# Kernel tuning notes

Measured on AMD Instinct MI355X. Metric: run time of the kernel, lower is better.

The kernel has to match this reference:

```python
import jax, jax.numpy as jnp
import numpy as np

N_NODES = 100000
N_EDGES = 1600000
IN_DIM, HID_DIM, OUT_DIM = 256, 128, 64


def setup_inputs() -> dict:
    key = jax.random.key(0)
    k1, k2, k3, k4, k5 = jax.random.split(key, 5)
    h = jax.random.normal(k1, (N_NODES, IN_DIM), dtype=jnp.float32)
    src = jax.random.randint(k2, (N_EDGES,), 0, N_NODES, dtype=jnp.int32)
    dst = jax.random.randint(k3, (N_EDGES,), 0, N_NODES, dtype=jnp.int32)
    # Glorot-uniform weights like DGL GraphConv defaults, zero bias
    lim1 = np.sqrt(6.0 / (IN_DIM + HID_DIM))
    lim2 = np.sqrt(6.0 / (HID_DIM + OUT_DIM))
    W1 = jax.random.uniform(k4, (IN_DIM, HID_DIM), jnp.float32, -lim1, lim1)
    W2 = jax.random.uniform(k5, (HID_DIM, OUT_DIM), jnp.float32, -lim2, lim2)
    b1 = jnp.zeros((HID_DIM,), jnp.float32)
    b2 = jnp.zeros((OUT_DIM,), jnp.float32)
    return {"h": h, "W1": W1, "b1": b1, "W2": W2, "b2": b2, "src": src, "dst": dst}


def _graph_conv(h, W, b, src, dst):
    # DGL GraphConv, norm='both', allow_zero_in_degree=True:
    #   out = D_in^{-1/2} A D_out^{-1/2} h W + b  (degrees clamped to min 1)
    ones = jnp.ones(src.shape[0], dtype=h.dtype)
    deg_out = jnp.clip(jax.ops.segment_sum(ones, src, num_segments=N_NODES), 1.0, None)
    feat = h * (deg_out ** -0.5)[:, None]
    # in_feats > out_feats for both layers -> multiply by W first (DGL order)
    feat = feat @ W  # [N, out]
    agg = jax.ops.segment_sum(feat[src], dst, num_segments=N_NODES)  # SpMM
    deg_in = jnp.clip(jax.ops.segment_sum(ones, dst, num_segments=N_NODES), 1.0, None)
    return agg * (deg_in ** -0.5)[:, None] + b


def reference(h, W1, b1, W2, b2, src, dst):
    # dropout is identity in eval mode (training=False)
    x = _graph_conv(h, W1, b1, src, dst)
    x = jax.nn.relu(x)
    logits = _graph_conv(x, W2, b2, src, dst)
    return jax.nn.softmax(logits, axis=1), logits
```

## Files before the change

kernel.cpp:

```cpp
#include <hip/hip_runtime.h>
#include <cstdio>

#define NN 100000
#define NE 1600000
#define IN_DIM 256
#define HID_DIM 128
#define OUT_DIM 64

#define EPB 4096
#define NBLK ((NE + EPB - 1) / EPB)
#define FBSH 7
#define FBN 128
#define NFB 782
#define CAP 2560
#define PREP_ELEMS (HID_DIM * IN_DIM + OUT_DIM * HID_DIM)
#define PREP_BLKS ((PREP_ELEMS + 127) / 128)

typedef short s8v __attribute__((ext_vector_type(8)));
typedef float f4v __attribute__((ext_vector_type(4)));
typedef _Float16 h2v __attribute__((ext_vector_type(2)));
typedef unsigned u32x4 __attribute__((ext_vector_type(4)));
typedef unsigned short u16x4 __attribute__((ext_vector_type(4)));
typedef unsigned short u16x8 __attribute__((ext_vector_type(8)));

__device__ __forceinline__ unsigned short f2bf(float f) {
    unsigned u = __builtin_bit_cast(unsigned, f);
    u += 0x7FFFu + ((u >> 16) & 1u);
    return (unsigned short)(u >> 16);
}
__device__ __forceinline__ unsigned short f2h(float f) {
    return __builtin_bit_cast(unsigned short, (_Float16)f);
}
__device__ __forceinline__ h2v bch2(unsigned w) { return __builtin_bit_cast(h2v, w); }

__global__ __launch_bounds__(256) void scat1_kernel(const int* __restrict__ src,
                                                    const int* __restrict__ dst,
                                                    unsigned short* __restrict__ cnt2dD,
                                                    unsigned short* __restrict__ cnt2dS) {
    __shared__ unsigned hbD[NFB], hbS[NFB];
    const int t = threadIdx.x;
    for (int i = t; i < NFB; i += 256) { hbD[i] = 0u; hbS[i] = 0u; }
    __syncthreads();
    const int base = blockIdx.x * EPB;
    int n = NE - base; if (n > EPB) n = EPB;
    for (int i = t; i < n; i += 256) {
        atomicAdd(&hbD[dst[base + i] >> FBSH], 1u);
        atomicAdd(&hbS[src[base + i] >> FBSH], 1u);
    }
    __syncthreads();
    const size_t row = (size_t)blockIdx.x * NFB;
    for (int i = t; i < NFB; i += 256) {
        cnt2dD[row + i] = (unsigned short)hbD[i];
        cnt2dS[row + i] = (unsigned short)hbS[i];
    }
}

__global__ __launch_bounds__(128) void scanCprep_kernel(unsigned short* __restrict__ cnt2dD,
                                                        unsigned short* __restrict__ cnt2dS,
                                                        unsigned* __restrict__ btotD,
                                                        unsigned* __restrict__ btotS,
                                                        const float* __restrict__ W1,
                                                        const float* __restrict__ W2,
                                                        unsigned short* __restrict__ W1t,
                                                        unsigned short* __restrict__ W2t) {
    const int g = blockIdx.x;
    if (g >= 2 * NFB) {
        int i = (g - 2 * NFB) * 128 + threadIdx.x;
        if (i < HID_DIM * IN_DIM) {
            int n = i >> 8, k = i & 255;
            W1t[i] = f2bf(W1[k * HID_DIM + n]);
        } else if (i < PREP_ELEMS) {
            int m = i - HID_DIM * IN_DIM;
            int n = m >> 7, k = m & 127;
            W2t[m] = f2bf(W2[k * OUT_DIM + n]);
        }
        return;
    }
    __shared__ unsigned sc[128];
    unsigned short* arr = (g < NFB) ? cnt2dD : cnt2dS;
    unsigned* btot = (g < NFB) ? btotD : btotS;
    const int b = (g < NFB) ? g : g - NFB;
    const int t = threadIdx.x;
    unsigned v[4];
    unsigned s = 0;
#pragma unroll
    for (int i = 0; i < 4; ++i) {
        int blk = t * 4 + i;
        unsigned x = (blk < NBLK) ? (unsigned)arr[(size_t)blk * NFB + b] : 0u;
        v[i] = s;
        s += x;
    }
    sc[t] = s;
    __syncthreads();
    for (int o = 1; o < 128; o <<= 1) {
        unsigned add = (t >= o) ? sc[t - o] : 0u;
        __syncthreads();
        sc[t] += add;
        __syncthreads();
    }
    unsigned incl = sc[t];
    unsigned excl = incl - s;
#pragma unroll
    for (int i = 0; i < 4; ++i) {
        int blk = t * 4 + i;
        if (blk < NBLK) arr[(size_t)blk * NFB + b] = (unsigned short)(excl + v[i]);
    }
    if (t == 127) btot[b] = incl;
}

__global__ __launch_bounds__(256) void scat2_kernel(const int* __restrict__ src,
                                                    const int* __restrict__ dst,
                                                    const unsigned short* __restrict__ ofsD,
                                                    const unsigned short* __restrict__ ofsS,
                                                    unsigned* __restrict__ ebufD,
                                                    unsigned char* __restrict__ ebufS) {
    __shared__ unsigned curD[NFB], curS[NFB];
    const int t = threadIdx.x;
    const size_t row = (size_t)blockIdx.x * NFB;
    for (int i = t; i < NFB; i += 256) {
        curD[i] = (unsigned)i * CAP + (unsigned)ofsD[row + i];
        curS[i] = (unsigned)i * CAP + (unsigned)ofsS[row + i];
    }
    __syncthreads();
    const int base = blockIdx.x * EPB;
    int n = NE - base; if (n > EPB) n = EPB;
    for (int i = t; i < n; i += 256) {
        int d = dst[base + i];
        int s = src[base + i];
        unsigned pD = atomicAdd(&curD[d >> FBSH], 1u);
        ebufD[pD] = ((unsigned)(d & 127) << 17) | (unsigned)s;
        unsigned pS = atomicAdd(&curS[s >> FBSH], 1u);
        ebufS[pS] = (unsigned char)(s & 127);
    }
}

__global__ __launch_bounds__(256) void bsortc_kernel(const unsigned* __restrict__ ebufD,
                                                     const unsigned* __restrict__ btotD,
                                                     const unsigned char* __restrict__ ebufS,
                                                     const unsigned* __restrict__ btotS,
                                                     int* __restrict__ csr,
                                                     unsigned* __restrict__ rsinfo,
                                                     float* __restrict__ dsin,
                                                     unsigned* __restrict__ cnt_out) {
    __shared__ unsigned hn[FBN];
    __shared__ unsigned sc[FBN];
    __shared__ unsigned cur[FBN];
    const int b = blockIdx.x;
    const int t = threadIdx.x;
    const unsigned e0 = (unsigned)b * CAP;
    const unsigned e1 = e0 + btotD[b];
    if (t < FBN) hn[t] = 0u;
    __syncthreads();
    for (unsigned j = e0 + t; j < e1; j += 256) atomicAdd(&hn[(ebufD[j] >> 17) & 127u], 1u);
    __syncthreads();
    unsigned cnt_t = (t < FBN) ? hn[t] : 0u;
    if (t < FBN) sc[t] = cnt_t;
    __syncthreads();
    for (int o = 1; o < FBN; o <<= 1) {
        unsigned add = (t < FBN && t >= o) ? sc[t - o] : 0u;
        __syncthreads();
        if (t < FBN) sc[t] += add;
        __syncthreads();
    }
    if (t < FBN) {
        unsigned excl = sc[t] - cnt_t;
        cur[t] = e0 + excl;
        int node = (b << FBSH) + t;
        if (node < NN) {
            rsinfo[node] = ((e0 + excl) << 10) | (cnt_t & 1023u);
            dsin[node] = rsqrtf((float)(cnt_t ? cnt_t : 1u));
        }
    }
    __syncthreads();
    for (unsigned j = e0 + t; j < e1; j += 256) {
        unsigned pk = ebufD[j];
        unsigned pos = atomicAdd(&cur[(pk >> 17) & 127u], 1u);
        csr[pos] = (int)(pk & 0x1FFFFu);
    }
    __syncthreads();
    if (t < FBN) hn[t] = 0u;
    __syncthreads();
    const unsigned nS = btotS[b];
    for (unsigned j = t; j < nS; j += 256) atomicAdd(&hn[ebufS[e0 + j]], 1u);
    __syncthreads();
    if (t < FBN) {
        int node = (b << FBSH) + t;
        if (node < NN) cnt_out[node] = hn[t];
    }
}

__global__ __launch_bounds__(256) void gemm1_kernel(const float* __restrict__ h,
                                                    const unsigned short* __restrict__ W1t,
                                                    const unsigned* __restrict__ cnt_out,
                                                    unsigned short* __restrict__ feat1, int M) {
    __shared__ unsigned short sA[2][128][40];
    const int tid = threadIdx.x;
    const int lane = tid & 63;
    const int wave = tid >> 6;
    const int wm = wave >> 1, wn = wave & 1;
    const int m0 = blockIdx.x * 128;
    const int arow = tid >> 3;
    const int akq = tid & 7;

    f4v acc[4][4];
#pragma unroll
    for (int i = 0; i < 4; ++i)
#pragma unroll
        for (int j = 0; j < 4; ++j) acc[i][j] = (f4v)0.f;

    int mrow[4]; bool mok[4];
#pragma unroll
    for (int i = 0; i < 4; ++i) { mrow[i] = m0 + arow + i * 32; mok[i] = mrow[i] < M; }

    float4 pre[4];
#pragma unroll
    for (int i = 0; i < 4; ++i)
        pre[i] = mok[i] ? *reinterpret_cast<const float4*>(&h[(size_t)mrow[i] * IN_DIM + akq * 4])
                        : make_float4(0.f, 0.f, 0.f, 0.f);
#pragma unroll
    for (int i = 0; i < 4; ++i) {
        u16x4 p;
        p[0] = f2bf(pre[i].x); p[1] = f2bf(pre[i].y);
        p[2] = f2bf(pre[i].z); p[3] = f2bf(pre[i].w);
        *reinterpret_cast<u16x4*>(&sA[0][arow + i * 32][akq * 4]) = p;
    }
    __syncthreads();

    int cur = 0;
#pragma unroll
    for (int ks = 0; ks < 8; ++ks) {
        if (ks < 7) {
            const int k0n = (ks + 1) * 32;
#pragma unroll
            for (int i = 0; i < 4; ++i)
                pre[i] = mok[i] ? *reinterpret_cast<const float4*>(
                                      &h[(size_t)mrow[i] * IN_DIM + k0n + akq * 4])
                                : make_float4(0.f, 0.f, 0.f, 0.f);
        }
        s8v bfrag[4];
#pragma unroll
        for (int ni = 0; ni < 4; ++ni)
            bfrag[ni] = *reinterpret_cast<const s8v*>(
                &W1t[(size_t)(wn * 64 + ni * 16 + (lane & 15)) * IN_DIM + ks * 32 + (lane >> 4) * 8]);
        s8v afrag[4];
#pragma unroll
        for (int mi = 0; mi < 4; ++mi)
            afrag[mi] = *reinterpret_cast<const s8v*>(
                &sA[cur][wm * 64 + mi * 16 + (lane & 15)][(lane >> 4) * 8]);
#pragma unroll
        for (int ni = 0; ni < 4; ++ni)
#pragma unroll
            for (int mi = 0; mi < 4; ++mi)
                acc[mi][ni] = __builtin_amdgcn_mfma_f32_16x16x32_bf16(afrag[mi], bfrag[ni], acc[mi][ni], 0, 0, 0);
        if (ks < 7) {
#pragma unroll
            for (int i = 0; i < 4; ++i) {
                u16x4 p;
                p[0] = f2bf(pre[i].x); p[1] = f2bf(pre[i].y);
                p[2] = f2bf(pre[i].z); p[3] = f2bf(pre[i].w);
                *reinterpret_cast<u16x4*>(&sA[cur ^ 1][arow + i * 32][akq * 4]) = p;
            }
        }
        __syncthreads();
        cur ^= 1;
    }
#pragma unroll
    for (int mi = 0; mi < 4; ++mi) {
#pragma unroll
        for (int j = 0; j < 4; ++j) {
            int row = m0 + wm * 64 + mi * 16 + (lane >> 4) * 4 + j;
            if (row < M) {
                unsigned cdeg = cnt_out[row];
                float s = rsqrtf((float)(cdeg ? cdeg : 1u));
#pragma unroll
                for (int ni = 0; ni < 4; ++ni) {
                    int col = wn * 64 + ni * 16 + (lane & 15);
                    feat1[(size_t)row * HID_DIM + col] = f2h(acc[mi][ni][j] * s);
                }
            }
        }
    }
}

__global__ __launch_bounds__(256) void gemm2_kernel(const unsigned short* __restrict__ xs,
                                                    const unsigned short* __restrict__ W2t,
                                                    unsigned short* __restrict__ feat2, int M) {
    __shared__ unsigned short sA[2][128][40];
    const int tid = threadIdx.x;
    const int lane = tid & 63;
    const int wave = tid >> 6;
    const int wm = wave >> 1, wn = wave & 1;
    const int m0 = blockIdx.x * 128;

    f4v acc[4][2];
#pragma unroll
    for (int i = 0; i < 4; ++i)
#pragma unroll
        for (int j = 0; j < 2; ++j) acc[i][j] = (f4v)0.f;

    int srow[2], skq[2]; bool sok[2];
#pragma unroll
    for (int i = 0; i < 2; ++i) {
        int idx = tid + i * 256;
        srow[i] = idx >> 2; skq[i] = idx & 3;
        sok[i] = (m0 + srow[i]) < M;
    }

    u16x8 pre[2];
#pragma unroll
    for (int i = 0; i < 2; ++i)
        pre[i] = sok[i] ? *reinterpret_cast<const u16x8*>(
                              &xs[(size_t)(m0 + srow[i]) * HID_DIM + skq[i] * 8])
                        : (u16x8)0;
#pragma unroll
    for (int i = 0; i < 2; ++i)
        *reinterpret_cast<u16x8*>(&sA[0][srow[i]][skq[i] * 8]) = pre[i];
    __syncthreads();

    int cur = 0;
#pragma unroll
    for (int ks = 0; ks < 4; ++ks) {
        if (ks < 3) {
            const int k0n = (ks + 1) * 32;
#pragma unroll
            for (int i = 0; i < 2; ++i)
                pre[i] = sok[i] ? *reinterpret_cast<const u16x8*>(
                                      &xs[(size_t)(m0 + srow[i]) * HID_DIM + k0n + skq[i] * 8])
                                : (u16x8)0;
        }
        s8v bfrag[2];
#pragma unroll
        for (int ni = 0; ni < 2; ++ni)
            bfrag[ni] = *reinterpret_cast<const s8v*>(
                &W2t[(size_t)(wn * 32 + ni * 16 + (lane & 15)) * HID_DIM + ks * 32 + (lane >> 4) * 8]);
        s8v afrag[4];
#pragma unroll
        for (int mi = 0; mi < 4; ++mi)
            afrag[mi] = *reinterpret_cast<const s8v*>(
                &sA[cur][wm * 64 + mi * 16 + (lane & 15)][(lane >> 4) * 8]);
#pragma unroll
        for (int ni = 0; ni < 2; ++ni)
#pragma unroll
            for (int mi = 0; mi < 4; ++mi)
                acc[mi][ni] = __builtin_amdgcn_mfma_f32_16x16x32_bf16(afrag[mi], bfrag[ni], acc[mi][ni], 0, 0, 0);
        if (ks < 3) {
#pragma unroll
            for (int i = 0; i < 2; ++i)
                *reinterpret_cast<u16x8*>(&sA[cur ^ 1][srow[i]][skq[i] * 8]) = pre[i];
        }
        __syncthreads();
        cur ^= 1;
    }
#pragma unroll
    for (int mi = 0; mi < 4; ++mi)
#pragma unroll
        for (int ni = 0; ni < 2; ++ni) {
            int col = wn * 32 + ni * 16 + (lane & 15);
#pragma unroll
            for (int j = 0; j < 4; ++j) {
                int row = m0 + wm * 64 + mi * 16 + (lane >> 4) * 4 + j;
                if (row < M) feat2[(size_t)row * OUT_DIM + col] = f2h(acc[mi][ni][j]);
            }
        }
}

__global__ __launch_bounds__(256) void spmm1_kernel(const unsigned short* __restrict__ feat,
                                                    const int* __restrict__ csr,
                                                    const unsigned* __restrict__ rsinfo,
                                                    const float* __restrict__ dsin,
                                                    const unsigned* __restrict__ cnt_out,
                                                    const float* __restrict__ b1,
                                                    unsigned short* __restrict__ xs) {
    const int wave = threadIdx.x >> 6;
    const int lane = threadIdx.x & 63;
    const int node = blockIdx.x * 4 + wave;
    if (node >= NN) return;
    const unsigned info = rsinfo[node];
    unsigned j = info >> 10;
    int rem = (int)(info & 1023u);
    const int g = lane >> 4;
    const int c8 = (lane & 15) * 8;
    h2v acch[4];
#pragma unroll
    for (int i = 0; i < 4; ++i) acch[i] = (h2v)0;
    while (rem > 0) {
        const int take = rem < 64 ? rem : 64;
        const int idx = (lane < take) ? csr[j + lane] : 0;
        int e = 0;
        for (; e + 16 <= take; e += 16) {
            int s0 = __shfl(idx, e + g, 64);
            int s1 = __shfl(idx, e + 4 + g, 64);
            int s2 = __shfl(idx, e + 8 + g, 64);
            int s3 = __shfl(idx, e + 12 + g, 64);
            u32x4 v0 = *reinterpret_cast<const u32x4*>(&feat[(size_t)s0 * HID_DIM + c8]);
            u32x4 v1 = *reinterpret_cast<const u32x4*>(&feat[(size_t)s1 * HID_DIM + c8]);
            u32x4 v2 = *reinterpret_cast<const u32x4*>(&feat[(size_t)s2 * HID_DIM + c8]);
            u32x4 v3 = *reinterpret_cast<const u32x4*>(&feat[(size_t)s3 * HID_DIM + c8]);
#pragma unroll
            for (int k = 0; k < 4; ++k) {
                h2v t0 = bch2(v0[k]) + bch2(v1[k]);
                h2v t1 = bch2(v2[k]) + bch2(v3[k]);
                acch[k] += t0 + t1;
            }
        }
        for (; e + 4 <= take; e += 4) {
            int s0 = __shfl(idx, e + g, 64);
            u32x4 v0 = *reinterpret_cast<const u32x4*>(&feat[(size_t)s0 * HID_DIM + c8]);
#pragma unroll
            for (int k = 0; k < 4; ++k) acch[k] += bch2(v0[k]);
        }
        if (e < take) {
            int ei = e + g;
            int sl = ei < take ? ei : take - 1;
            int s0 = __shfl(idx, sl, 64);
            u32x4 v0 = *reinterpret_cast<const u32x4*>(&feat[(size_t)s0 * HID_DIM + c8]);
            if (ei < take) {
#pragma unroll
                for (int k = 0; k < 4; ++k) acch[k] += bch2(v0[k]);
            }
        }
        j += take; rem -= take;
    }
#pragma unroll
    for (int k = 0; k < 4; ++k) {
        unsigned w = __builtin_bit_cast(unsigned, acch[k]);
        acch[k] += bch2((unsigned)__shfl_xor((int)w, 16, 64));
        w = __builtin_bit_cast(unsigned, acch[k]);
        acch[k] += bch2((unsigned)__shfl_xor((int)w, 32, 64));
    }
    if (g == 0) {
        const float si = dsin[node];
        const unsigned co = cnt_out[node];
        const float so = rsqrtf((float)(co ? co : 1u));
        const float4 bb0 = *reinterpret_cast<const float4*>(&b1[c8]);
        const float4 bb1 = *reinterpret_cast<const float4*>(&b1[c8 + 4]);
        const float bv[8] = {bb0.x, bb0.y, bb0.z, bb0.w, bb1.x, bb1.y, bb1.z, bb1.w};
        u16x8 p;
#pragma unroll
        for (int k = 0; k < 4; ++k) {
            p[2 * k] = f2bf(fmaxf((float)acch[k][0] * si + bv[2 * k], 0.f) * so);
            p[2 * k + 1] = f2bf(fmaxf((float)acch[k][1] * si + bv[2 * k + 1], 0.f) * so);
        }
        *reinterpret_cast<u16x8*>(&xs[(size_t)node * HID_DIM + c8]) = p;
    }
}

__global__ __launch_bounds__(256) void spmm2_kernel(const unsigned short* __restrict__ feat2,
                                                    const int* __restrict__ csr,
                                                    const unsigned* __restrict__ rsinfo,
                                                    const float* __restrict__ dsin,
                                                    const float* __restrict__ b2,
                                                    float* __restrict__ out) {
    const int wave = threadIdx.x >> 6;
    const int lane = threadIdx.x & 63;
    const int node = blockIdx.x * 4 + wave;
    if (node >= NN) return;
    const unsigned info = rsinfo[node];
    unsigned j = info >> 10;
    int rem = (int)(info & 1023u);
    const int g = lane >> 3;
    const int c8 = (lane & 7) * 8;
    h2v acch[4];
#pragma unroll
    for (int i = 0; i < 4; ++i) acch[i] = (h2v)0;
    while (rem > 0) {
        const int take = rem < 64 ? rem : 64;
        const int idx = (lane < take) ? csr[j + lane] : 0;
        int e = 0;
        for (; e + 32 <= take; e += 32) {
            int s0 = __shfl(idx, e + g, 64);
            int s1 = __shfl(idx, e + 8 + g, 64);
            int s2 = __shfl(idx, e + 16 + g, 64);
            int s3 = __shfl(idx, e + 24 + g, 64);
            u32x4 v0 = *reinterpret_cast<const u32x4*>(&feat2[(size_t)s0 * OUT_DIM + c8]);
            u32x4 v1 = *reinterpret_cast<const u32x4*>(&feat2[(size_t)s1 * OUT_DIM + c8]);
            u32x4 v2 = *reinterpret_cast<const u32x4*>(&feat2[(size_t)s2 * OUT_DIM + c8]);
            u32x4 v3 = *reinterpret_cast<const u32x4*>(&feat2[(size_t)s3 * OUT_DIM + c8]);
#pragma unroll
            for (int k = 0; k < 4; ++k) {
                h2v t0 = bch2(v0[k]) + bch2(v1[k]);
                h2v t1 = bch2(v2[k]) + bch2(v3[k]);
                acch[k] += t0 + t1;
            }
        }
        for (; e + 16 <= take; e += 16) {
            int s0 = __shfl(idx, e + g, 64);
            int s1 = __shfl(idx, e + 8 + g, 64);
            u32x4 v0 = *reinterpret_cast<const u32x4*>(&feat2[(size_t)s0 * OUT_DIM + c8]);
            u32x4 v1 = *reinterpret_cast<const u32x4*>(&feat2[(size_t)s1 * OUT_DIM + c8]);
#pragma unroll
            for (int k = 0; k < 4; ++k) acch[k] += bch2(v0[k]) + bch2(v1[k]);
        }
        for (; e + 8 <= take; e += 8) {
            int s0 = __shfl(idx, e + g, 64);
            u32x4 v0 = *reinterpret_cast<const u32x4*>(&feat2[(size_t)s0 * OUT_DIM + c8]);
#pragma unroll
            for (int k = 0; k < 4; ++k) acch[k] += bch2(v0[k]);
        }
        if (e < take) {
            int ei = e + g;
            int sl = ei < take ? ei : take - 1;
            int s0 = __shfl(idx, sl, 64);
            u32x4 v0 = *reinterpret_cast<const u32x4*>(&feat2[(size_t)s0 * OUT_DIM + c8]);
            if (ei < take) {
#pragma unroll
                for (int k = 0; k < 4; ++k) acch[k] += bch2(v0[k]);
            }
        }
        j += take; rem -= take;
    }
#pragma unroll
    for (int k = 0; k < 4; ++k) {
        unsigned w = __builtin_bit_cast(unsigned, acch[k]);
        acch[k] += bch2((unsigned)__shfl_xor((int)w, 8, 64));
        w = __builtin_bit_cast(unsigned, acch[k]);
        acch[k] += bch2((unsigned)__shfl_xor((int)w, 16, 64));
        w = __builtin_bit_cast(unsigned, acch[k]);
        acch[k] += bch2((unsigned)__shfl_xor((int)w, 32, 64));
    }
    const float si = dsin[node];
    const float4 bb0 = *reinterpret_cast<const float4*>(&b2[c8]);
    const float4 bb1 = *reinterpret_cast<const float4*>(&b2[c8 + 4]);
    const float bv[8] = {bb0.x, bb0.y, bb0.z, bb0.w, bb1.x, bb1.y, bb1.z, bb1.w};
    float l[8];
#pragma unroll
    for (int k = 0; k < 4; ++k) {
        l[2 * k] = (float)acch[k][0] * si + bv[2 * k];
        l[2 * k + 1] = (float)acch[k][1] * si + bv[2 * k + 1];
    }
    float m = l[0];
#pragma unroll
    for (int i = 1; i < 8; ++i) m = fmaxf(m, l[i]);
    m = fmaxf(m, __shfl_xor(m, 1, 64));
    m = fmaxf(m, __shfl_xor(m, 2, 64));
    m = fmaxf(m, __shfl_xor(m, 4, 64));
    float ee[8];
    float s = 0.f;
#pragma unroll
    for (int i = 0; i < 8; ++i) { ee[i] = __expf(l[i] - m); s += ee[i]; }
    s += __shfl_xor(s, 1, 64);
    s += __shfl_xor(s, 2, 64);
    s += __shfl_xor(s, 4, 64);
    const float inv = 1.0f / s;
    if (lane < 8) {
        float4 p0 = make_float4(ee[0] * inv, ee[1] * inv, ee[2] * inv, ee[3] * inv);
        float4 p1 = make_float4(ee[4] * inv, ee[5] * inv, ee[6] * inv, ee[7] * inv);
        *reinterpret_cast<float4*>(&out[(size_t)node * OUT_DIM + c8]) = p0;
        *reinterpret_cast<float4*>(&out[(size_t)node * OUT_DIM + c8 + 4]) = p1;
        float4 q0 = make_float4(l[0], l[1], l[2], l[3]);
        float4 q1 = make_float4(l[4], l[5], l[6], l[7]);
        float* lg = &out[(size_t)NN * OUT_DIM + (size_t)node * OUT_DIM + c8];
        *reinterpret_cast<float4*>(lg) = q0;
        *reinterpret_cast<float4*>(lg + 4) = q1;
    }
}

static inline size_t align_up(size_t x, size_t a) { return (x + a - 1) & ~(a - 1); }

extern "C" void kernel_launch(void* const* d_in, const int* in_sizes, int n_in,
                              void* d_out, int out_size, void* d_ws, size_t ws_size,
                              hipStream_t stream) {
    (void)in_sizes; (void)n_in; (void)out_size;
    const float* h = (const float*)d_in[0];
    const float* W1 = (const float*)d_in[1];
    const float* b1 = (const float*)d_in[2];
    const float* W2 = (const float*)d_in[3];
    const float* b2 = (const float*)d_in[4];
    const int* src = (const int*)d_in[5];
    const int* dst = (const int*)d_in[6];
    float* out = (float*)d_out;

    char* ws = (char*)d_ws;
    size_t off = 0;
    auto alloc = [&](size_t bytes) {
        void* p = (void*)(ws + off);
        off = align_up(off + bytes, 512);
        return p;
    };
    unsigned* cnt_out = (unsigned*)alloc(NN * 4);
    unsigned short* cnt2dD = (unsigned short*)alloc((size_t)NBLK * NFB * 2);
    unsigned short* cnt2dS = (unsigned short*)alloc((size_t)NBLK * NFB * 2);
    unsigned* btotD = (unsigned*)alloc(NFB * 4);
    unsigned* btotS = (unsigned*)alloc(NFB * 4);
    unsigned* rsinfo = (unsigned*)alloc(NN * 4);
    float* dsin = (float*)alloc(NN * 4);
    unsigned* ebufD = (unsigned*)alloc((size_t)NFB * CAP * 4);
    unsigned char* ebufS = (unsigned char*)alloc((size_t)NFB * CAP);
    int* csr = (int*)alloc((size_t)NFB * CAP * 4);
    unsigned short* W1t = (unsigned short*)alloc((size_t)HID_DIM * IN_DIM * 2);
    unsigned short* W2t = (unsigned short*)alloc((size_t)OUT_DIM * HID_DIM * 2);
    unsigned short* feat1 = (unsigned short*)alloc((size_t)NN * HID_DIM * 2);
    unsigned short* xs = (unsigned short*)alloc((size_t)NN * HID_DIM * 2);
    unsigned short* feat2 = feat1;

    if (off > ws_size) {
        fprintf(stderr, "kernel_launch: ws too small: need %zu, have %zu\n", off, ws_size);
        return;
    }

    scat1_kernel<<<NBLK, 256, 0, stream>>>(src, dst, cnt2dD, cnt2dS);
    scanCprep_kernel<<<2 * NFB + PREP_BLKS, 128, 0, stream>>>(cnt2dD, cnt2dS, btotD, btotS,
                                                              W1, W2, W1t, W2t);
    scat2_kernel<<<NBLK, 256, 0, stream>>>(src, dst, cnt2dD, cnt2dS, ebufD, ebufS);
    bsortc_kernel<<<NFB, 256, 0, stream>>>(ebufD, btotD, ebufS, btotS, csr, rsinfo, dsin,
                                           cnt_out);

    gemm1_kernel<<<(NN + 127) / 128, 256, 0, stream>>>(h, W1t, cnt_out, feat1, NN);
    spmm1_kernel<<<(NN + 3) / 4, 256, 0, stream>>>(feat1, csr, rsinfo, dsin, cnt_out, b1, xs);
    gemm2_kernel<<<(NN + 127) / 128, 256, 0, stream>>>(xs, W2t, feat2, NN);
    spmm2_kernel<<<(NN + 3) / 4, 256, 0, stream>>>(feat2, csr, rsinfo, dsin, b2, out);
}
```

Before: 218.7 us.

## Store hidden features in column-sliced layout so SpMM1 gathers stay cache-resident

Feat1 and xs move from row-major [N,128] to 8 slices of [N,16] fp16/bf16 columns, and gemm1, spmm1 and gemm2 are updated to that layout. Each spmm1 block now handles one 16-column slice for 8 nodes, with half-waves gathering 32-byte segments per edge. Blocks with the same slice index share a 3.2MB working set, which is meant to improve L2/MALL hit rates on the random gathers. The costs are 8x more blocks, each re-reading CSR indices and degree data, smaller 32-byte gather transactions, and an extra reduction step across lanes.

```diff
diff --git a/kernel.cpp b/kernel.cpp
--- a/kernel.cpp
+++ b/kernel.cpp
@@ -27,6 +27,10 @@
     unsigned u = __builtin_bit_cast(unsigned, f);
     u += 0x7FFFu + ((u >> 16) & 1u);
     return (unsigned short)(u >> 16);
+}
+__device__ __forceinline__ float bf2f(unsigned short s) {
+    unsigned u = ((unsigned)s) << 16;
+    return __builtin_bit_cast(float, u);
 }
 __device__ __forceinline__ unsigned short f2h(float f) {
     return __builtin_bit_cast(unsigned short, (_Float16)f);
@@ -274,8 +278,9 @@
                 float s = rsqrtf((float)(cdeg ? cdeg : 1u));
 #pragma unroll
                 for (int ni = 0; ni < 4; ++ni) {
-                    int col = wn * 64 + ni * 16 + (lane & 15);
-                    feat1[(size_t)row * HID_DIM + col] = f2h(acc[mi][ni][j] * s);
+                    int slice = wn * 4 + ni;
+                    feat1[((size_t)slice * NN + row) * 16 + (lane & 15)] =
+                        f2h(acc[mi][ni][j] * s);
                 }
             }
         }
@@ -310,7 +315,8 @@
 #pragma unroll
     for (int i = 0; i < 2; ++i)
         pre[i] = sok[i] ? *reinterpret_cast<const u16x8*>(
-                              &xs[(size_t)(m0 + srow[i]) * HID_DIM + skq[i] * 8])
+                              &xs[((size_t)(skq[i] >> 1) * NN + (m0 + srow[i])) * 16 +
+                                  (skq[i] & 1) * 8])
                         : (u16x8)0;
 #pragma unroll
     for (int i = 0; i < 2; ++i)
@@ -321,11 +327,11 @@
 #pragma unroll
     for (int ks = 0; ks < 4; ++ks) {
         if (ks < 3) {
-            const int k0n = (ks + 1) * 32;
 #pragma unroll
             for (int i = 0; i < 2; ++i)
                 pre[i] = sok[i] ? *reinterpret_cast<const u16x8*>(
-                                      &xs[(size_t)(m0 + srow[i]) * HID_DIM + k0n + skq[i] * 8])
+                                      &xs[((size_t)(2 * (ks + 1) + (skq[i] >> 1)) * NN +
+                                           (m0 + srow[i])) * 16 + (skq[i] & 1) * 8])
                                 : (u16x8)0;
         }
         s8v bfrag[2];
@@ -371,77 +377,59 @@
                                                     const unsigned* __restrict__ cnt_out,
                                                     const float* __restrict__ b1,
                                                     unsigned short* __restrict__ xs) {
-    const int wave = threadIdx.x >> 6;
-    const int lane = threadIdx.x & 63;
-    const int node = blockIdx.x * 4 + wave;
-    if (node >= NN) return;
-    const unsigned info = rsinfo[node];
+    const int tid = threadIdx.x;
+    const int wave = tid >> 6;
+    const int lane = tid & 63;
+    const int s = blockIdx.x & 7;
+    const int grp = blockIdx.x >> 3;
+    const int h = lane >> 5;
+    const int node = grp * 8 + wave * 2 + h;
+    const unsigned short* fs = feat + (size_t)s * NN * 16;
+    const bool ok = node < NN;
+    unsigned info = ok ? rsinfo[node] : 0u;
     unsigned j = info >> 10;
     int rem = (int)(info & 1023u);
-    const int g = lane >> 4;
-    const int c8 = (lane & 15) * 8;
-    h2v acch[4];
-#pragma unroll
-    for (int i = 0; i < 4; ++i) acch[i] = (h2v)0;
-    while (rem > 0) {
-        const int take = rem < 64 ? rem : 64;
-        const int idx = (lane < take) ? csr[j + lane] : 0;
-        int e = 0;
-        for (; e + 16 <= take; e += 16) {
-            int s0 = __shfl(idx, e + g, 64);
-            int s1 = __shfl(idx, e + 4 + g, 64);
-            int s2 = __shfl(idx, e + 8 + g, 64);
-            int s3 = __shfl(idx, e + 12 + g, 64);
-            u32x4 v0 = *reinterpret_cast<const u32x4*>(&feat[(size_t)s0 * HID_DIM + c8]);
-            u32x4 v1 = *reinterpret_cast<const u32x4*>(&feat[(size_t)s1 * HID_DIM + c8]);
-            u32x4 v2 = *reinterpret_cast<const u32x4*>(&feat[(size_t)s2 * HID_DIM + c8]);
-            u32x4 v3 = *reinterpret_cast<const u32x4*>(&feat[(size_t)s3 * HID_DIM + c8]);
-#pragma unroll
-            for (int k = 0; k < 4; ++k) {
-                h2v t0 = bch2(v0[k]) + bch2(v1[k]);
-                h2v t1 = bch2(v2[k]) + bch2(v3[k]);
-                acch[k] += t0 + t1;
-            }
-        }
-        for (; e + 4 <= take; e += 4) {
-            int s0 = __shfl(idx, e + g, 64);
-            u32x4 v0 = *reinterpret_cast<const u32x4*>(&feat[(size_t)s0 * HID_DIM + c8]);
-#pragma unroll
-            for (int k = 0; k < 4; ++k) acch[k] += bch2(v0[k]);
-        }
-        if (e < take) {
-            int ei = e + g;
-            int sl = ei < take ? ei : take - 1;
-            int s0 = __shfl(idx, sl, 64);
-            u32x4 v0 = *reinterpret_cast<const u32x4*>(&feat[(size_t)s0 * HID_DIM + c8]);
-            if (ei < take) {
-#pragma unroll
-                for (int k = 0; k < 4; ++k) acch[k] += bch2(v0[k]);
-            }
+    const int slot = (lane & 31) >> 1;
+    const int hw = lane & 1;
+    h2v acc[4];
+#pragma unroll
+    for (int k = 0; k < 4; ++k) acc[k] = (h2v)0;
+    while (__any(rem > 0)) {
+        int take = rem < 16 ? rem : 16;
+        if (slot < take) {
+            int srcn = csr[j + slot];
+            u32x4 v = *reinterpret_cast<const u32x4*>(&fs[(size_t)srcn * 16 + hw * 8]);
+#pragma unroll
+            for (int k = 0; k < 4; ++k) acc[k] += bch2(v[k]);
         }
         j += take; rem -= take;
     }
 #pragma unroll
     for (int k = 0; k < 4; ++k) {
-        unsigned w = __builtin_bit_cast(unsigned, acch[k]);
-        acch[k] += bch2((unsigned)__shfl_xor((int)w, 16, 64));
-        w = __builtin_bit_cast(unsigned, acch[k]);
-        acch[k] += bch2((unsigned)__shfl_xor((int)w, 32, 64));
-    }
-    if (g == 0) {
+        unsigned w = __builtin_bit_cast(unsigned, acc[k]);
+        acc[k] += bch2((unsigned)__shfl_xor((int)w, 2, 64));
+        w = __builtin_bit_cast(unsigned, acc[k]);
+        acc[k] += bch2((unsigned)__shfl_xor((int)w, 4, 64));
+        w = __builtin_bit_cast(unsigned, acc[k]);
+        acc[k] += bch2((unsigned)__shfl_xor((int)w, 8, 64));
+        w = __builtin_bit_cast(unsigned, acc[k]);
+        acc[k] += bch2((unsigned)__shfl_xor((int)w, 16, 64));
+    }
+    if ((lane & 31) < 2 && ok) {
         const float si = dsin[node];
         const unsigned co = cnt_out[node];
         const float so = rsqrtf((float)(co ? co : 1u));
-        const float4 bb0 = *reinterpret_cast<const float4*>(&b1[c8]);
-        const float4 bb1 = *reinterpret_cast<const float4*>(&b1[c8 + 4]);
+        const int d0 = s * 16 + hw * 8;
+        const float4 bb0 = *reinterpret_cast<const float4*>(&b1[d0]);
+        const float4 bb1 = *reinterpret_cast<const float4*>(&b1[d0 + 4]);
         const float bv[8] = {bb0.x, bb0.y, bb0.z, bb0.w, bb1.x, bb1.y, bb1.z, bb1.w};
         u16x8 p;
 #pragma unroll
         for (int k = 0; k < 4; ++k) {
-            p[2 * k] = f2bf(fmaxf((float)acch[k][0] * si + bv[2 * k], 0.f) * so);
-            p[2 * k + 1] = f2bf(fmaxf((float)acch[k][1] * si + bv[2 * k + 1], 0.f) * so);
-        }
-        *reinterpret_cast<u16x8*>(&xs[(size_t)node * HID_DIM + c8]) = p;
+            p[2 * k] = f2bf(fmaxf((float)acc[k][0] * si + bv[2 * k], 0.f) * so);
+            p[2 * k + 1] = f2bf(fmaxf((float)acc[k][1] * si + bv[2 * k + 1], 0.f) * so);
+        }
+        *reinterpret_cast<u16x8*>(&xs[((size_t)s * NN + node) * 16 + hw * 8]) = p;
     }
 }
 
@@ -606,7 +594,8 @@
                                            cnt_out);
 
     gemm1_kernel<<<(NN + 127) / 128, 256, 0, stream>>>(h, W1t, cnt_out, feat1, NN);
-    spmm1_kernel<<<(NN + 3) / 4, 256, 0, stream>>>(feat1, csr, rsinfo, dsin, cnt_out, b1, xs);
+    spmm1_kernel<<<((NN + 7) / 8) * 8, 256, 0, stream>>>(feat1, csr, rsinfo, dsin, cnt_out,
+                                                         b1, xs);
     gemm2_kernel<<<(NN + 127) / 128, 256, 0, stream>>>(xs, W2t, feat2, NN);
     spmm2_kernel<<<(NN + 3) / 4, 256, 0, stream>>>(feat2, csr, rsinfo, dsin, b2, out);
 }
```

Result: slower. 288.7 us (+32.0%).
